# Performance work log

Hardware: AMD Instinct MI355X
Metric: run time of the kernel (lower is better)

## Reference

```python
import jax, jax.numpy as jnp
import numpy as np

N_NODES = 100000
N_EDGES = 1600000
D_IN = 64
D_HID = 64
N_LAYERS = 3


def setup_inputs() -> dict:
    key = jax.random.key(0)
    ks = jax.random.split(key, 10)
    inp = {
        "node_feat": jax.random.normal(ks[0], (N_NODES, D_IN), dtype=jnp.float32),
        "src": jax.random.randint(ks[1], (N_EDGES,), 0, N_NODES, dtype=jnp.int32),
        "dst": jax.random.randint(ks[2], (N_EDGES,), 0, N_NODES, dtype=jnp.int32),
        "graph_len": jnp.ones((1,), dtype=jnp.int32) * N_NODES,
    }
    # GraphConv weights: shape (in_feats, out_feats), applied as feat @ W + b (DGL xavier-style init)
    dims = [D_IN] + [D_HID] * N_LAYERS
    for i in range(N_LAYERS):
        scale = float(np.sqrt(2.0 / (dims[i] + dims[i + 1])))
        inp[f"W{i}"] = jax.random.normal(ks[3 + i], (dims[i], dims[i + 1]), dtype=jnp.float32) * scale
        inp[f"b{i}"] = jnp.zeros((dims[i + 1],), dtype=jnp.float32)
    return inp


def reference(node_feat, src, dst, graph_len, W0, b0, W1, b1, W2, b2):
    n = node_feat.shape[0]
    e = src.shape[0]
    ones = jnp.ones((e,), dtype=node_feat.dtype)
    # DGL GraphConv norm='both': src-side out-degree^{-1/2}, dst-side in-degree^{-1/2}, clamp(min=1)
    deg_out = jax.ops.segment_sum(ones, src, num_segments=n)
    deg_in = jax.ops.segment_sum(ones, dst, num_segments=n)
    inv_sqrt_out = jax.lax.rsqrt(jnp.clip(deg_out, 1.0, None))[:, None]  # [N,1]
    inv_sqrt_in = jax.lax.rsqrt(jnp.clip(deg_in, 1.0, None))[:, None]    # [N,1]

    def graph_conv(x, W, b):
        msg = (x * inv_sqrt_out)[src]                              # [E,F] gather
        agg = jax.ops.segment_sum(msg, dst, num_segments=n)        # [N,F] scatter-add
        return (agg * inv_sqrt_in) @ W + b                         # SpMM result -> dense linear

    xs = []
    h = node_feat
    for W, b in ((W0, b0), (W1, b1), (W2, b2)):
        h = jax.nn.relu(graph_conv(h, W, b))
        xs.append(h)

    # Faithful to source: torch.sum(x, dim=1) -> per-node scalar [N]; concat over layers -> [3N]
    x_pool = jnp.concatenate([x.sum(axis=1) for x in xs], axis=-1)
    xs_cat = jnp.concatenate(xs, axis=-1)  # [N, 3*H]
    return x_pool, xs_cat
```

## Files before the change

### kernel.cpp

```cpp
#include <hip/hip_runtime.h>


#define CAPB 8192
#define CAP_S2 5120
#define CPAD 16

__device__ __forceinline__ unsigned short f2bf(float f) {
  unsigned u = __float_as_uint(f);
  u += 0x7fff + ((u >> 16) & 1);
  return (unsigned short)(u >> 16);
}
__device__ __forceinline__ float bflo(unsigned u) { return __uint_as_float(u << 16); }
__device__ __forceinline__ float bfhi(unsigned u) { return __uint_as_float(u & 0xffff0000u); }

__global__ void init_zero(int* __restrict__ cur_d, int* __restrict__ cur_s) {
  int idx = blockIdx.x * 256 + threadIdx.x;
  if (idx < 512 * CPAD) {
    int v = (idx % CPAD == 0) ? (idx / CPAD) * CAPB : 0;
    cur_d[idx] = v;
    cur_s[idx] = v;
  }
}

__global__ __launch_bounds__(1024) void scatter_both(
    const int* __restrict__ src, const int* __restrict__ dst, int e,
    int* __restrict__ cur_d, int* __restrict__ cur_s,
    unsigned* __restrict__ edges1, unsigned char* __restrict__ srcbuf) {
  __shared__ int stW[4096], stG[4096];
  __shared__ int hist[512], curL[512], gofs[512], psum[512];
  int t = threadIdx.x, b = blockIdx.x;
  int i0 = b * 4096 + 4 * t;
  int sv[4], dv[4];
  if (i0 + 3 < e) {
    int4 s4 = *(const int4*)&src[i0];
    int4 d4 = *(const int4*)&dst[i0];
    sv[0] = s4.x; sv[1] = s4.y; sv[2] = s4.z; sv[3] = s4.w;
    dv[0] = d4.x; dv[1] = d4.y; dv[2] = d4.z; dv[3] = d4.w;
  } else {
    #pragma unroll
    for (int j = 0; j < 4; j++) {
      int idx = i0 + j;
      if (idx < e) { sv[j] = src[idx]; dv[j] = dst[idx]; }
      else { sv[j] = -1; dv[j] = -1; }
    }
  }
  if (t < 512) hist[t] = 0;
  __syncthreads();
  #pragma unroll
  for (int k = 0; k < 4; k++)
    if (dv[k] >= 0) atomicAdd(&hist[dv[k] >> 8], 1);
  __syncthreads();
  if (t < 512) psum[t] = hist[t];
  __syncthreads();
  for (int off = 1; off < 512; off <<= 1) {
    int a = 0;
    if (t < 512 && t >= off) a = psum[t - off];
    __syncthreads();
    if (t < 512) psum[t] += a;
    __syncthreads();
  }
  if (t < 512) {
    int cnt = hist[t];
    int base = psum[t] - cnt;
    curL[t] = base;
    int g = cnt ? atomicAdd(&cur_d[t * CPAD], cnt) : 0;
    gofs[t] = g - base;
  }
  __syncthreads();
  #pragma unroll
  for (int k = 0; k < 4; k++) {
    if (dv[k] >= 0) {
      int bin = dv[k] >> 8;
      int r = atomicAdd(&curL[bin], 1);
      stW[r] = (sv[k] << 8) | (dv[k] & 255);
      stG[r] = gofs[bin] + r;
    }
  }
  __syncthreads();
  int tot = psum[511];
  for (int idx = t; idx < tot; idx += 1024)
    edges1[stG[idx]] = (unsigned)stW[idx];
  __syncthreads();
  if (t < 512) hist[t] = 0;
  __syncthreads();
  #pragma unroll
  for (int k = 0; k < 4; k++)
    if (dv[k] >= 0) atomicAdd(&hist[sv[k] >> 8], 1);
  __syncthreads();
  if (t < 512) psum[t] = hist[t];
  __syncthreads();
  for (int off = 1; off < 512; off <<= 1) {
    int a = 0;
    if (t < 512 && t >= off) a = psum[t - off];
    __syncthreads();
    if (t < 512) psum[t] += a;
    __syncthreads();
  }
  if (t < 512) {
    int cnt = hist[t];
    int base = psum[t] - cnt;
    curL[t] = base;
    int g = cnt ? atomicAdd(&cur_s[t * CPAD], cnt) : 0;
    gofs[t] = g - base;
  }
  __syncthreads();
  #pragma unroll
  for (int k = 0; k < 4; k++) {
    if (dv[k] >= 0) {
      int bin = sv[k] >> 8;
      int r = atomicAdd(&curL[bin], 1);
      stW[r] = sv[k] & 255;
      stG[r] = gofs[bin] + r;
    }
  }
  __syncthreads();
  for (int idx = t; idx < tot; idx += 1024)
    srcbuf[stG[idx]] = (unsigned char)stW[idx];
}

__global__ __launch_bounds__(512) void sort_place(
    const unsigned* __restrict__ edges1, const unsigned char* __restrict__ srcbuf,
    const int* __restrict__ cur_d, const int* __restrict__ cur_s,
    int2* __restrict__ row_be, float* __restrict__ inv_in, float* __restrict__ inv_out,
    int* __restrict__ col, int n) {
  __shared__ int sOut[CAP_S2];
  __shared__ int hist[256], cur[256], psum[256], dhist[256];
  int b = blockIdx.x, t = threadIdx.x;
  int sbase = b * CAPB;
  int ed = cur_d[b * CPAD];
  int es = cur_s[b * CPAD];
  int rstart = b << 8;
  int nrows = min(256, n - rstart);
  if (t < 256) { hist[t] = 0; dhist[t] = 0; }
  __syncthreads();
  for (int i = sbase + t; i < ed; i += 512) atomicAdd(&hist[edges1[i] & 255u], 1);
  for (int i = sbase + t; i < es; i += 512) atomicAdd(&dhist[srcbuf[i]], 1);
  __syncthreads();
  int h0 = 0;
  if (t < 256) { h0 = hist[t]; psum[t] = h0; }
  __syncthreads();
  for (int off = 1; off < 256; off <<= 1) {
    int a = 0;
    if (t < 256 && t >= off) a = psum[t - off];
    __syncthreads();
    if (t < 256) psum[t] += a;
    __syncthreads();
  }
  if (t < 256) {
    int ex = psum[t] - h0;
    if (t < nrows) {
      row_be[rstart + t] = make_int2(sbase + ex, sbase + ex + h0);
      inv_in[rstart + t] = rsqrtf(fmaxf((float)h0, 1.0f));
      inv_out[rstart + t] = rsqrtf(fmaxf((float)dhist[t], 1.0f));
    }
    cur[t] = ex;
  }
  __syncthreads();
  for (int i = sbase + t; i < ed; i += 512) {
    unsigned v = edges1[i];
    int pos = atomicAdd(&cur[v & 255u], 1);
    int svv = (int)(v >> 8);
    if (pos < CAP_S2) sOut[pos] = svv;
    else col[sbase + pos] = svv;
  }
  __syncthreads();
  int m = min(ed - sbase, CAP_S2);
  for (int k = t; k < m; k += 512) col[sbase + k] = sOut[k];
}

__global__ __launch_bounds__(256) void cast_xb(
    const float* __restrict__ node_feat, const float* __restrict__ inv_out,
    unsigned short* __restrict__ xb, int n) {
  int total4 = n * 16;
  int stride = gridDim.x * 256;
  for (int u = blockIdx.x * 256 + threadIdx.x; u < total4; u += stride) {
    int r = u >> 4;
    float iv = inv_out[r];
    float4 v = *(const float4*)&node_feat[(size_t)u * 4];
    ushort4 o;
    o.x = f2bf(v.x * iv); o.y = f2bf(v.y * iv);
    o.z = f2bf(v.z * iv); o.w = f2bf(v.w * iv);
    *(ushort4*)&xb[(size_t)u * 4] = o;
  }
}

__global__ __launch_bounds__(512) void spmm_gemm(
    const unsigned short* __restrict__ xb,
    const int2* __restrict__ row_be,
    const int* __restrict__ col,
    const float* __restrict__ inv_in, const float* __restrict__ inv_out,
    const float* __restrict__ W, const float* __restrict__ bias,
    float* __restrict__ out_cat, float* __restrict__ out_pool,
    unsigned short* __restrict__ xb_next, int n) {
  __shared__ float sXT[64][68];
  int t = threadIdx.x;
  int row0 = blockIdx.x << 6;
  int lane = t & 63;
  int g = lane >> 3;
  int l8 = (lane & 7) << 3;
  int wv = t >> 6;
  for (int k = 0; k < 8; k++) {
    int rl = wv * 8 + k;
    int row = row0 + rl;
    float v = 0.f;
    if (row < n) {
      int2 be = row_be[row];
      int s = be.x, e = be.y;
      float inv = inv_in[row];
      float a0 = 0, a1 = 0, a2 = 0, a3 = 0, a4 = 0, a5 = 0, a6 = 0, a7 = 0;
      int ec = e - 1;
      for (int i = s + g; i < e; i += 16) {
        int i1 = i + 8;
        int c0 = col[i];
        int c1 = col[min(i1, ec)];
        float m1 = (i1 < e) ? 1.f : 0.f;
        uint4 r0 = *(const uint4*)&xb[(size_t)c0 * 64 + l8];
        uint4 r1 = *(const uint4*)&xb[(size_t)c1 * 64 + l8];
        a0 += bflo(r0.x); a1 += bfhi(r0.x); a2 += bflo(r0.y); a3 += bfhi(r0.y);
        a4 += bflo(r0.z); a5 += bfhi(r0.z); a6 += bflo(r0.w); a7 += bfhi(r0.w);
        a0 = fmaf(m1, bflo(r1.x), a0); a1 = fmaf(m1, bfhi(r1.x), a1);
        a2 = fmaf(m1, bflo(r1.y), a2); a3 = fmaf(m1, bfhi(r1.y), a3);
        a4 = fmaf(m1, bflo(r1.z), a4); a5 = fmaf(m1, bfhi(r1.z), a5);
        a6 = fmaf(m1, bflo(r1.w), a6); a7 = fmaf(m1, bfhi(r1.w), a7);
      }
      a0 += __shfl_xor(a0, 8); a0 += __shfl_xor(a0, 16); a0 += __shfl_xor(a0, 32);
      a1 += __shfl_xor(a1, 8); a1 += __shfl_xor(a1, 16); a1 += __shfl_xor(a1, 32);
      a2 += __shfl_xor(a2, 8); a2 += __shfl_xor(a2, 16); a2 += __shfl_xor(a2, 32);
      a3 += __shfl_xor(a3, 8); a3 += __shfl_xor(a3, 16); a3 += __shfl_xor(a3, 32);
      a4 += __shfl_xor(a4, 8); a4 += __shfl_xor(a4, 16); a4 += __shfl_xor(a4, 32);
      a5 += __shfl_xor(a5, 8); a5 += __shfl_xor(a5, 16); a5 += __shfl_xor(a5, 32);
      a6 += __shfl_xor(a6, 8); a6 += __shfl_xor(a6, 16); a6 += __shfl_xor(a6, 32);
      a7 += __shfl_xor(a7, 8); a7 += __shfl_xor(a7, 16); a7 += __shfl_xor(a7, 32);
      float s0 = (g & 1) ? a1 : a0;
      float s1 = (g & 1) ? a3 : a2;
      float s2 = (g & 1) ? a5 : a4;
      float s3 = (g & 1) ? a7 : a6;
      float u0 = (g & 2) ? s1 : s0;
      float u1 = (g & 2) ? s3 : s2;
      v = ((g & 4) ? u1 : u0) * inv;
    }
    sXT[l8 + g][rl] = v;
  }
  __syncthreads();
  int tj = t & 15, tr = t >> 4;
  int j4 = tj << 2, r2 = tr << 1;
  const float4 bv = *(const float4*)&bias[j4];
  float4 a0 = bv, a1 = bv;
  #pragma unroll 8
  for (int f = 0; f < 64; f++) {
    float4 w  = *(const float4*)&W[f * 64 + j4];
    float2 xv = *(const float2*)&sXT[f][r2];
    a0.x = fmaf(xv.x, w.x, a0.x); a0.y = fmaf(xv.x, w.y, a0.y);
    a0.z = fmaf(xv.x, w.z, a0.z); a0.w = fmaf(xv.x, w.w, a0.w);
    a1.x = fmaf(xv.y, w.x, a1.x); a1.y = fmaf(xv.y, w.y, a1.y);
    a1.z = fmaf(xv.y, w.z, a1.z); a1.w = fmaf(xv.y, w.w, a1.w);
  }
  float4 accs[2] = {a0, a1};
  #pragma unroll
  for (int ri = 0; ri < 2; ri++) {
    int row = row0 + r2 + ri;
    if (row < n) {
      float4 h = accs[ri];
      h.x = fmaxf(h.x, 0.f); h.y = fmaxf(h.y, 0.f);
      h.z = fmaxf(h.z, 0.f); h.w = fmaxf(h.w, 0.f);
      *(float4*)&out_cat[(size_t)row * 192 + j4] = h;
      if (xb_next) {
        float sc = inv_out[row];
        ushort4 o;
        o.x = f2bf(h.x * sc); o.y = f2bf(h.y * sc);
        o.z = f2bf(h.z * sc); o.w = f2bf(h.w * sc);
        *(ushort4*)&xb_next[(size_t)row * 64 + j4] = o;
      }
      float part = h.x + h.y + h.z + h.w;
      part += __shfl_xor(part, 1);
      part += __shfl_xor(part, 2);
      part += __shfl_xor(part, 4);
      part += __shfl_xor(part, 8);
      if (tj == 0) out_pool[row] = part;
    }
  }
}


extern "C" void kernel_launch(void* const* d_in, const int* in_sizes, int n_in,
                              void* d_out, int out_size, void* d_ws, size_t ws_size,
                              hipStream_t stream) {
  const float* node_feat = (const float*)d_in[0];
  const int* src = (const int*)d_in[1];
  const int* dst = (const int*)d_in[2];
  const float* Ws[3] = {(const float*)d_in[4], (const float*)d_in[6], (const float*)d_in[8]};
  const float* bs[3] = {(const float*)d_in[5], (const float*)d_in[7], (const float*)d_in[9]};
  float* out = (float*)d_out;
  int n = in_sizes[0] / 64;
  int e = in_sizes[1];
  int nbb = (n + 255) >> 8;
  int nblk = (e + 4095) / 4096;
  size_t slots = (size_t)nbb * CAPB;

  char* p = (char*)d_ws;
  unsigned short* xba = (unsigned short*)p; p += (size_t)n * 64 * sizeof(unsigned short);
  unsigned short* xbb = (unsigned short*)p; p += (size_t)n * 64 * sizeof(unsigned short);
  float* inv_out = (float*)p;   p += (size_t)n * sizeof(float);
  float* inv_in = (float*)p;    p += (size_t)n * sizeof(float);
  int2* row_be = (int2*)p;      p += (size_t)n * sizeof(int2);
  int* cur_d = (int*)p;         p += 512 * CPAD * sizeof(int);
  int* cur_s = (int*)p;         p += 512 * CPAD * sizeof(int);
  unsigned* edges1 = (unsigned*)p; p += slots * sizeof(unsigned);
  int* col = (int*)p;           p += slots * sizeof(int);
  unsigned char* srcbuf = (unsigned char*)p; p += slots;

  init_zero<<<32, 256, 0, stream>>>(cur_d, cur_s);
  scatter_both<<<nblk, 1024, 0, stream>>>(src, dst, e, cur_d, cur_s, edges1, srcbuf);
  sort_place<<<nbb, 512, 0, stream>>>(edges1, srcbuf, cur_d, cur_s,
                                      row_be, inv_in, inv_out, col, n);
  cast_xb<<<1024, 256, 0, stream>>>(node_feat, inv_out, xba, n);

  float* cat_base = out + (size_t)3 * n;
  int nfb = (n + 63) >> 6;
  spmm_gemm<<<nfb, 512, 0, stream>>>(xba, row_be, col, inv_in, inv_out,
      Ws[0], bs[0], cat_base + 0 * 64, out + (size_t)0 * n, xbb, n);
  spmm_gemm<<<nfb, 512, 0, stream>>>(xbb, row_be, col, inv_in, inv_out,
      Ws[1], bs[1], cat_base + 1 * 64, out + (size_t)1 * n, xba, n);
  spmm_gemm<<<nfb, 512, 0, stream>>>(xba, row_be, col, inv_in, inv_out,
      Ws[2], bs[2], cat_base + 2 * 64, out + (size_t)2 * n, (unsigned short*)nullptr, n);
}
```

Baseline: 345.8 us.

## Use 128-node buckets, stage edges in LDS, fuse bf16 cast into sort_place

Bucket width drops from 256 to 128 nodes, so the scatter pass uses 1024 bins and each sort_place block handles a smaller bucket. Each bucket's edges are loaded into shared memory once and reused for both the histogram and the placement, and the spill path to global memory is removed. The separate cast_xb kernel is folded into sort_place, which now scales and converts its own 128 feature rows, saving a launch and a reread of inv_out. In exchange the scatter pass does a longer 1024-entry scan and writes more global atomics. A bucket with more than 4096 edges would overflow the new capacity, since the overflow path is gone.

Result: slower. 355.7 us (+2.9%).

```diff
diff --git a/kernel.cpp b/kernel.cpp
--- a/kernel.cpp
+++ b/kernel.cpp
@@ -1,8 +1,7 @@
 #include <hip/hip_runtime.h>
 
 
-#define CAPB 8192
-#define CAP_S2 5120
+#define CAPB 4096
 #define CPAD 16
 
 __device__ __forceinline__ unsigned short f2bf(float f) {
@@ -15,7 +14,7 @@
 
 __global__ void init_zero(int* __restrict__ cur_d, int* __restrict__ cur_s) {
   int idx = blockIdx.x * 256 + threadIdx.x;
-  if (idx < 512 * CPAD) {
+  if (idx < 1024 * CPAD) {
     int v = (idx % CPAD == 0) ? (idx / CPAD) * CAPB : 0;
     cur_d[idx] = v;
     cur_s[idx] = v;
@@ -27,7 +26,7 @@
     int* __restrict__ cur_d, int* __restrict__ cur_s,
     unsigned* __restrict__ edges1, unsigned char* __restrict__ srcbuf) {
   __shared__ int stW[4096], stG[4096];
-  __shared__ int hist[512], curL[512], gofs[512], psum[512];
+  __shared__ int hist[1024], curL[1024], gofs[1024], psum[1024];
   int t = threadIdx.x, b = blockIdx.x;
   int i0 = b * 4096 + 4 * t;
   int sv[4], dv[4];
@@ -44,22 +43,21 @@
       else { sv[j] = -1; dv[j] = -1; }
     }
   }
-  if (t < 512) hist[t] = 0;
+  hist[t] = 0;
   __syncthreads();
   #pragma unroll
   for (int k = 0; k < 4; k++)
-    if (dv[k] >= 0) atomicAdd(&hist[dv[k] >> 8], 1);
-  __syncthreads();
-  if (t < 512) psum[t] = hist[t];
-  __syncthreads();
-  for (int off = 1; off < 512; off <<= 1) {
-    int a = 0;
-    if (t < 512 && t >= off) a = psum[t - off];
-    __syncthreads();
-    if (t < 512) psum[t] += a;
-    __syncthreads();
-  }
-  if (t < 512) {
+    if (dv[k] >= 0) atomicAdd(&hist[dv[k] >> 7], 1);
+  __syncthreads();
+  psum[t] = hist[t];
+  __syncthreads();
+  for (int off = 1; off < 1024; off <<= 1) {
+    int a = (t >= off) ? psum[t - off] : 0;
+    __syncthreads();
+    psum[t] += a;
+    __syncthreads();
+  }
+  {
     int cnt = hist[t];
     int base = psum[t] - cnt;
     curL[t] = base;
@@ -70,33 +68,32 @@
   #pragma unroll
   for (int k = 0; k < 4; k++) {
     if (dv[k] >= 0) {
-      int bin = dv[k] >> 8;
+      int bin = dv[k] >> 7;
       int r = atomicAdd(&curL[bin], 1);
-      stW[r] = (sv[k] << 8) | (dv[k] & 255);
+      stW[r] = (sv[k] << 7) | (dv[k] & 127);
       stG[r] = gofs[bin] + r;
     }
   }
   __syncthreads();
-  int tot = psum[511];
+  int tot = psum[1023];
   for (int idx = t; idx < tot; idx += 1024)
     edges1[stG[idx]] = (unsigned)stW[idx];
   __syncthreads();
-  if (t < 512) hist[t] = 0;
+  hist[t] = 0;
   __syncthreads();
   #pragma unroll
   for (int k = 0; k < 4; k++)
-    if (dv[k] >= 0) atomicAdd(&hist[sv[k] >> 8], 1);
-  __syncthreads();
-  if (t < 512) psum[t] = hist[t];
-  __syncthreads();
-  for (int off = 1; off < 512; off <<= 1) {
-    int a = 0;
-    if (t < 512 && t >= off) a = psum[t - off];
-    __syncthreads();
-    if (t < 512) psum[t] += a;
-    __syncthreads();
-  }
-  if (t < 512) {
+    if (dv[k] >= 0) atomicAdd(&hist[sv[k] >> 7], 1);
+  __syncthreads();
+  psum[t] = hist[t];
+  __syncthreads();
+  for (int off = 1; off < 1024; off <<= 1) {
+    int a = (t >= off) ? psum[t - off] : 0;
+    __syncthreads();
+    psum[t] += a;
+    __syncthreads();
+  }
+  {
     int cnt = hist[t];
     int base = psum[t] - cnt;
     curL[t] = base;
@@ -107,9 +104,9 @@
   #pragma unroll
   for (int k = 0; k < 4; k++) {
     if (dv[k] >= 0) {
-      int bin = sv[k] >> 8;
+      int bin = sv[k] >> 7;
       int r = atomicAdd(&curL[bin], 1);
-      stW[r] = sv[k] & 255;
+      stW[r] = sv[k] & 127;
       stG[r] = gofs[bin] + r;
     }
   }
@@ -121,66 +118,65 @@
 __global__ __launch_bounds__(512) void sort_place(
     const unsigned* __restrict__ edges1, const unsigned char* __restrict__ srcbuf,
     const int* __restrict__ cur_d, const int* __restrict__ cur_s,
+    const float* __restrict__ node_feat,
     int2* __restrict__ row_be, float* __restrict__ inv_in, float* __restrict__ inv_out,
-    int* __restrict__ col, int n) {
-  __shared__ int sOut[CAP_S2];
-  __shared__ int hist[256], cur[256], psum[256], dhist[256];
+    unsigned short* __restrict__ xb, int* __restrict__ col, int n) {
+  __shared__ int sEdge[CAPB];
+  __shared__ int sOut[CAPB];
+  __shared__ int hist[128], cur[128], psum[128], dhist[128];
+  __shared__ float sInvO[128];
   int b = blockIdx.x, t = threadIdx.x;
   int sbase = b * CAPB;
-  int ed = cur_d[b * CPAD];
-  int es = cur_s[b * CPAD];
-  int rstart = b << 8;
-  int nrows = min(256, n - rstart);
-  if (t < 256) { hist[t] = 0; dhist[t] = 0; }
-  __syncthreads();
-  for (int i = sbase + t; i < ed; i += 512) atomicAdd(&hist[edges1[i] & 255u], 1);
-  for (int i = sbase + t; i < es; i += 512) atomicAdd(&dhist[srcbuf[i]], 1);
+  int m = cur_d[b * CPAD] - sbase;
+  int ms = cur_s[b * CPAD] - sbase;
+  int rstart = b << 7;
+  int nrows = min(128, n - rstart);
+  if (t < 128) { hist[t] = 0; dhist[t] = 0; }
+  __syncthreads();
+  for (int k = t; k < m; k += 512) sEdge[k] = (int)edges1[sbase + k];
+  for (int k = t; k < ms; k += 512) atomicAdd(&dhist[srcbuf[sbase + k]], 1);
+  __syncthreads();
+  for (int k = t; k < m; k += 512) atomicAdd(&hist[sEdge[k] & 127], 1);
   __syncthreads();
   int h0 = 0;
-  if (t < 256) { h0 = hist[t]; psum[t] = h0; }
-  __syncthreads();
-  for (int off = 1; off < 256; off <<= 1) {
+  if (t < 128) { h0 = hist[t]; psum[t] = h0; }
+  __syncthreads();
+  for (int off = 1; off < 128; off <<= 1) {
     int a = 0;
-    if (t < 256 && t >= off) a = psum[t - off];
-    __syncthreads();
-    if (t < 256) psum[t] += a;
-    __syncthreads();
-  }
-  if (t < 256) {
+    if (t < 128 && t >= off) a = psum[t - off];
+    __syncthreads();
+    if (t < 128) psum[t] += a;
+    __syncthreads();
+  }
+  if (t < 128) {
     int ex = psum[t] - h0;
+    float ivo = rsqrtf(fmaxf((float)dhist[t], 1.0f));
+    sInvO[t] = ivo;
     if (t < nrows) {
       row_be[rstart + t] = make_int2(sbase + ex, sbase + ex + h0);
       inv_in[rstart + t] = rsqrtf(fmaxf((float)h0, 1.0f));
-      inv_out[rstart + t] = rsqrtf(fmaxf((float)dhist[t], 1.0f));
+      inv_out[rstart + t] = ivo;
     }
     cur[t] = ex;
   }
   __syncthreads();
-  for (int i = sbase + t; i < ed; i += 512) {
-    unsigned v = edges1[i];
-    int pos = atomicAdd(&cur[v & 255u], 1);
-    int svv = (int)(v >> 8);
-    if (pos < CAP_S2) sOut[pos] = svv;
-    else col[sbase + pos] = svv;
-  }
-  __syncthreads();
-  int m = min(ed - sbase, CAP_S2);
+  for (int k = t; k < m; k += 512) {
+    int v = sEdge[k];
+    int pos = atomicAdd(&cur[v & 127], 1);
+    sOut[pos] = v >> 7;
+  }
+  __syncthreads();
   for (int k = t; k < m; k += 512) col[sbase + k] = sOut[k];
-}
-
-__global__ __launch_bounds__(256) void cast_xb(
-    const float* __restrict__ node_feat, const float* __restrict__ inv_out,
-    unsigned short* __restrict__ xb, int n) {
-  int total4 = n * 16;
-  int stride = gridDim.x * 256;
-  for (int u = blockIdx.x * 256 + threadIdx.x; u < total4; u += stride) {
-    int r = u >> 4;
-    float iv = inv_out[r];
-    float4 v = *(const float4*)&node_feat[(size_t)u * 4];
+  int total4 = nrows * 16;
+  const float4* nf4 = (const float4*)(node_feat + (size_t)rstart * 64);
+  ushort4* xb4 = (ushort4*)(xb + (size_t)rstart * 64);
+  for (int u = t; u < total4; u += 512) {
+    float iv = sInvO[u >> 4];
+    float4 v = nf4[u];
     ushort4 o;
     o.x = f2bf(v.x * iv); o.y = f2bf(v.y * iv);
     o.z = f2bf(v.z * iv); o.w = f2bf(v.w * iv);
-    *(ushort4*)&xb[(size_t)u * 4] = o;
+    xb4[u] = o;
   }
 }
 
@@ -293,7 +289,7 @@
   float* out = (float*)d_out;
   int n = in_sizes[0] / 64;
   int e = in_sizes[1];
-  int nbb = (n + 255) >> 8;
+  int nbb = (n + 127) >> 7;
   int nblk = (e + 4095) / 4096;
   size_t slots = (size_t)nbb * CAPB;
 
@@ -303,17 +299,16 @@
   float* inv_out = (float*)p;   p += (size_t)n * sizeof(float);
   float* inv_in = (float*)p;    p += (size_t)n * sizeof(float);
   int2* row_be = (int2*)p;      p += (size_t)n * sizeof(int2);
-  int* cur_d = (int*)p;         p += 512 * CPAD * sizeof(int);
-  int* cur_s = (int*)p;         p += 512 * CPAD * sizeof(int);
+  int* cur_d = (int*)p;         p += 1024 * CPAD * sizeof(int);
+  int* cur_s = (int*)p;         p += 1024 * CPAD * sizeof(int);
   unsigned* edges1 = (unsigned*)p; p += slots * sizeof(unsigned);
   int* col = (int*)p;           p += slots * sizeof(int);
   unsigned char* srcbuf = (unsigned char*)p; p += slots;
 
-  init_zero<<<32, 256, 0, stream>>>(cur_d, cur_s);
+  init_zero<<<64, 256, 0, stream>>>(cur_d, cur_s);
   scatter_both<<<nblk, 1024, 0, stream>>>(src, dst, e, cur_d, cur_s, edges1, srcbuf);
-  sort_place<<<nbb, 512, 0, stream>>>(edges1, srcbuf, cur_d, cur_s,
-                                      row_be, inv_in, inv_out, col, n);
-  cast_xb<<<1024, 256, 0, stream>>>(node_feat, inv_out, xba, n);
+  sort_place<<<nbb, 512, 0, stream>>>(edges1, srcbuf, cur_d, cur_s, node_feat,
+                                      row_be, inv_in, inv_out, xba, col, n);
 
   float* cat_base = out + (size_t)3 * n;
   int nfb = (n + 63) >> 6;
```

## Split bf16 feature matrix into four 16-column planes for cache-friendly SpMM gathers

Applied to the files above, without the earlier changes.

The bf16 node feature buffer is stored as four column-chunk planes of 16 features (32 bytes per row per plane) instead of 64 contiguous features per row. The SpMM now makes four passes, one per plane, with each wave covering 16 edges per step and gathering 8-byte segments. The aim is to shrink each plane's working set so gathers hit in L2/MALL. In exchange, each row's edge list and column indices are read four times, the gathers are narrower, and the old two-edge unroll is gone.

Measured after the change: 552.5 us. +59.8%, slower.

```diff
diff --git a/kernel.cpp b/kernel.cpp
--- a/kernel.cpp
+++ b/kernel.cpp
@@ -10,8 +10,7 @@
   u += 0x7fff + ((u >> 16) & 1);
   return (unsigned short)(u >> 16);
 }
-__device__ __forceinline__ float bflo(unsigned u) { return __uint_as_float(u << 16); }
-__device__ __forceinline__ float bfhi(unsigned u) { return __uint_as_float(u & 0xffff0000u); }
+__device__ __forceinline__ float bfs(unsigned short s) { return __uint_as_float((unsigned)s << 16); }
 
 __global__ void init_zero(int* __restrict__ cur_d, int* __restrict__ cur_s) {
   int idx = blockIdx.x * 256 + threadIdx.x;
@@ -173,14 +172,15 @@
     unsigned short* __restrict__ xb, int n) {
   int total4 = n * 16;
   int stride = gridDim.x * 256;
+  const float4* nf4 = (const float4*)node_feat;
   for (int u = blockIdx.x * 256 + threadIdx.x; u < total4; u += stride) {
-    int r = u >> 4;
+    int r = u >> 4, c = u & 15;
     float iv = inv_out[r];
-    float4 v = *(const float4*)&node_feat[(size_t)u * 4];
+    float4 v = nf4[u];
     ushort4 o;
     o.x = f2bf(v.x * iv); o.y = f2bf(v.y * iv);
     o.z = f2bf(v.z * iv); o.w = f2bf(v.w * iv);
-    *(ushort4*)&xb[(size_t)u * 4] = o;
+    *(ushort4*)&xb[(((size_t)(c >> 2) * n + r) << 4) + ((c & 3) << 2)] = o;
   }
 }
 
@@ -196,50 +196,34 @@
   int t = threadIdx.x;
   int row0 = blockIdx.x << 6;
   int lane = t & 63;
-  int g = lane >> 3;
-  int l8 = (lane & 7) << 3;
+  int q4 = (lane & 3) << 2;
+  int eg = lane >> 2;
   int wv = t >> 6;
-  for (int k = 0; k < 8; k++) {
-    int rl = wv * 8 + k;
-    int row = row0 + rl;
-    float v = 0.f;
-    if (row < n) {
-      int2 be = row_be[row];
-      int s = be.x, e = be.y;
-      float inv = inv_in[row];
-      float a0 = 0, a1 = 0, a2 = 0, a3 = 0, a4 = 0, a5 = 0, a6 = 0, a7 = 0;
-      int ec = e - 1;
-      for (int i = s + g; i < e; i += 16) {
-        int i1 = i + 8;
-        int c0 = col[i];
-        int c1 = col[min(i1, ec)];
-        float m1 = (i1 < e) ? 1.f : 0.f;
-        uint4 r0 = *(const uint4*)&xb[(size_t)c0 * 64 + l8];
-        uint4 r1 = *(const uint4*)&xb[(size_t)c1 * 64 + l8];
-        a0 += bflo(r0.x); a1 += bfhi(r0.x); a2 += bflo(r0.y); a3 += bfhi(r0.y);
-        a4 += bflo(r0.z); a5 += bfhi(r0.z); a6 += bflo(r0.w); a7 += bfhi(r0.w);
-        a0 = fmaf(m1, bflo(r1.x), a0); a1 = fmaf(m1, bfhi(r1.x), a1);
-        a2 = fmaf(m1, bflo(r1.y), a2); a3 = fmaf(m1, bfhi(r1.y), a3);
-        a4 = fmaf(m1, bflo(r1.z), a4); a5 = fmaf(m1, bfhi(r1.z), a5);
-        a6 = fmaf(m1, bflo(r1.w), a6); a7 = fmaf(m1, bfhi(r1.w), a7);
+  for (int fc = 0; fc < 4; fc++) {
+    const unsigned short* xs = xb + ((size_t)fc * n << 4);
+    for (int k = 0; k < 8; k++) {
+      int rl = (wv << 3) + k;
+      int row = row0 + rl;
+      float val = 0.f;
+      if (row < n) {
+        int2 be = row_be[row];
+        float inv = inv_in[row];
+        float a0 = 0, a1 = 0, a2 = 0, a3 = 0;
+        for (int i = be.x + eg; i < be.y; i += 16) {
+          int c = col[i];
+          ushort4 u4 = *(const ushort4*)&xs[((size_t)c << 4) + q4];
+          a0 += bfs(u4.x); a1 += bfs(u4.y); a2 += bfs(u4.z); a3 += bfs(u4.w);
+        }
+        a0 += __shfl_xor(a0, 4); a0 += __shfl_xor(a0, 8); a0 += __shfl_xor(a0, 16); a0 += __shfl_xor(a0, 32);
+        a1 += __shfl_xor(a1, 4); a1 += __shfl_xor(a1, 8); a1 += __shfl_xor(a1, 16); a1 += __shfl_xor(a1, 32);
+        a2 += __shfl_xor(a2, 4); a2 += __shfl_xor(a2, 8); a2 += __shfl_xor(a2, 16); a2 += __shfl_xor(a2, 32);
+        a3 += __shfl_xor(a3, 4); a3 += __shfl_xor(a3, 8); a3 += __shfl_xor(a3, 16); a3 += __shfl_xor(a3, 32);
+        float s0 = (eg & 1) ? a1 : a0;
+        float s1 = (eg & 1) ? a3 : a2;
+        val = ((eg & 2) ? s1 : s0) * inv;
       }
-      a0 += __shfl_xor(a0, 8); a0 += __shfl_xor(a0, 16); a0 += __shfl_xor(a0, 32);
-      a1 += __shfl_xor(a1, 8); a1 += __shfl_xor(a1, 16); a1 += __shfl_xor(a1, 32);
-      a2 += __shfl_xor(a2, 8); a2 += __shfl_xor(a2, 16); a2 += __shfl_xor(a2, 32);
-      a3 += __shfl_xor(a3, 8); a3 += __shfl_xor(a3, 16); a3 += __shfl_xor(a3, 32);
-      a4 += __shfl_xor(a4, 8); a4 += __shfl_xor(a4, 16); a4 += __shfl_xor(a4, 32);
-      a5 += __shfl_xor(a5, 8); a5 += __shfl_xor(a5, 16); a5 += __shfl_xor(a5, 32);
-      a6 += __shfl_xor(a6, 8); a6 += __shfl_xor(a6, 16); a6 += __shfl_xor(a6, 32);
-      a7 += __shfl_xor(a7, 8); a7 += __shfl_xor(a7, 16); a7 += __shfl_xor(a7, 32);
-      float s0 = (g & 1) ? a1 : a0;
-      float s1 = (g & 1) ? a3 : a2;
-      float s2 = (g & 1) ? a5 : a4;
-      float s3 = (g & 1) ? a7 : a6;
-      float u0 = (g & 2) ? s1 : s0;
-      float u1 = (g & 2) ? s3 : s2;
-      v = ((g & 4) ? u1 : u0) * inv;
-    }
-    sXT[l8 + g][rl] = v;
+      if (eg < 4) sXT[(fc << 4) + q4 + eg][rl] = val;
+    }
   }
   __syncthreads();
   int tj = t & 15, tr = t >> 4;
@@ -269,7 +253,7 @@
         ushort4 o;
         o.x = f2bf(h.x * sc); o.y = f2bf(h.y * sc);
         o.z = f2bf(h.z * sc); o.w = f2bf(h.w * sc);
-        *(ushort4*)&xb_next[(size_t)row * 64 + j4] = o;
+        *(ushort4*)&xb_next[(((size_t)(tj >> 2) * n + row) << 4) + ((tj & 3) << 2)] = o;
       }
       float part = h.x + h.y + h.z + h.w;
       part += __shfl_xor(part, 1);
```
